# Kernel tuning notes

Hardware: AMD Instinct MI355X
Metric: run time of the kernel (lower is better)

Reference implementation:

```python
import jax, jax.numpy as jnp
import numpy as np

# ---- fixed wavelet filters (Selesnick FSfarras first-stage + Kingsbury Q-shift) ----
_F1 = np.array([
    [0.0, 0.0],
    [-0.08838834764832, -0.01122679215254],
    [0.08838834764832, 0.01122679215254],
    [0.69587998903400, 0.08838834764832],
    [0.69587998903400, 0.08838834764832],
    [0.08838834764832, -0.69587998903400],
    [-0.08838834764832, 0.69587998903400],
    [0.01122679215254, -0.08838834764832],
    [0.01122679215254, -0.08838834764832],
    [0.0, 0.0]], np.float32)
_F2 = np.array([
    [0.01122679215254, 0.0],
    [0.01122679215254, 0.0],
    [-0.08838834764832, -0.08838834764832],
    [0.08838834764832, -0.08838834764832],
    [0.69587998903400, 0.69587998903400],
    [0.69587998903400, -0.69587998903400],
    [0.08838834764832, 0.08838834764832],
    [-0.08838834764832, 0.08838834764832],
    [0.0, 0.01122679215254],
    [0.0, -0.01122679215254]], np.float32)
_Q1 = np.array([
    [0.03516384, 0.0],
    [0.0, 0.0],
    [-0.08832942, -0.11430184],
    [0.23389032, 0.0],
    [0.76027237, 0.58751830],
    [0.58751830, -0.76027237],
    [0.0, 0.23389032],
    [-0.11430184, 0.08832942],
    [0.0, 0.0],
    [0.0, -0.03516384]], np.float32)
_Q2 = np.array([
    [0.0, -0.03516384],
    [0.0, 0.0],
    [-0.11430184, 0.08832942],
    [0.0, 0.23389032],
    [0.58751830, -0.76027237],
    [0.76027237, 0.58751830],
    [0.23389032, 0.0],
    [-0.08832942, -0.11430184],
    [0.0, 0.0],
    [0.03516384, 0.0]], np.float32)
# synthesis filters are the time-reversed analysis filters
FSF = jnp.asarray(np.stack([_F1[::-1].copy(), _F2[::-1].copy()]))  # [2, 10, 2] first stage
SF = jnp.asarray(np.stack([_Q1[::-1].copy(), _Q2[::-1].copy()]))   # [2, 10, 2] Q-shift


def _upconv(x, f, axis):
    """Upsample-by-2 + full convolution with 1D filter f along `axis` (upfirdn(x,f,2,1))."""
    L = f.shape[0]
    xm = jnp.moveaxis(x, axis, -1)
    shp = xm.shape
    xr = xm.reshape(-1, 1, shp[-1])  # [M, 1, n] NCW
    k = f[::-1].astype(x.dtype).reshape(1, 1, L)  # flip -> true convolution
    y = jax.lax.conv_general_dilated(
        xr, k, window_strides=(1,), padding=[(L - 1, L - 1)],
        lhs_dilation=(2,), dimension_numbers=('NCW', 'OIW', 'NCW'))  # [M,1,2n+L-2]
    y = y.reshape(shp[:-1] + (y.shape[-1],))
    return jnp.moveaxis(y, -1, axis)


def sfb1d(lo, hi, sf, axis):
    """1D synthesis filter bank with periodic wrap + circular shift (Selesnick sfb1D)."""
    L = sf.shape[0]
    N = 2 * lo.shape[axis]
    y = _upconv(lo, sf[:, 0], axis) + _upconv(hi, sf[:, 1], axis)  # length N+L-2
    yN = jax.lax.slice_in_dim(y, 0, N, axis=axis)
    tail = jax.lax.slice_in_dim(y, N, N + L - 2, axis=axis)
    head = jax.lax.slice_in_dim(yN, 0, L - 2, axis=axis) + tail
    rest = jax.lax.slice_in_dim(yN, L - 2, N, axis=axis)
    return jnp.roll(jnp.concatenate([head, rest], axis=axis), 1 - L // 2, axis=axis)


def sfb2d(lo, hi3, sf_row, sf_col):
    """2D separable synthesis: hi3 = (LH, HL, HH); x is [B, H, W, C]."""
    lo = sfb1d(lo, hi3[0], sf_col, axis=2)
    h = sfb1d(hi3[1], hi3[2], sf_col, axis=2)
    return sfb1d(lo, h, sf_row, axis=1)


def _idtcwt(highs0, highs1, lows):
    inv_sqrt2 = jnp.asarray(1.0 / np.sqrt(2.0), highs0.dtype)

    def pm(a, b):
        return (a + b) * inv_sqrt2, (a - b) * inv_sqrt2

    # orientation butterflies per level (add_sub)
    wi = [[[[None] * 3 for _ in range(2)] for _ in range(2)] for _ in range(2)]
    for j, hj in enumerate((highs0, highs1)):
        for b in range(3):
            u, v = pm(hj[0, 0, b], hj[1, 1, b])
            wi[j][0][0][b], wi[j][1][1][b] = u, v
            u, v = pm(hj[0, 1, b], hj[1, 0, b])
            wi[j][0][1][b], wi[j][1][0][b] = u, v

    y = jnp.zeros_like(lows[0, 0], shape=(lows.shape[2], lows.shape[3] * 4,
                                          lows.shape[4] * 4, lows.shape[5]))
    for m in range(2):
        for n in range(2):
            lo = lows[m, n]
            lo = sfb2d(lo, wi[1][m][n], SF[m], SF[n])      # level 2 (Q-shift)
            lo = sfb2d(lo, wi[0][m][n], FSF[m], FSF[n])    # level 1 (first stage)
            y = y + lo
    return y / 2


def setup_inputs() -> dict:
    key = jax.random.key(0)
    k0, k1, k2 = jax.random.split(key, 3)
    B, C = 16, 3
    highs0 = jax.random.normal(k0, (2, 2, 3, B, 256, 256, C), dtype=jnp.float32)
    highs1 = jax.random.normal(k1, (2, 2, 3, B, 128, 128, C), dtype=jnp.float32)
    lows = jax.random.normal(k2, (2, 2, B, 128, 128, C), dtype=jnp.float32)
    return {"highs0": highs0, "highs1": highs1, "lows": lows}


def reference(highs0, highs1, lows):
    return _idtcwt(highs0, highs1, lows)
```

## Files before the change

kernel.cpp:

```cpp
#include <hip/hip_runtime.h>

#define INV_SQRT2 0.70710678118654752440f
#define KH 0.35355339059327376220f

constexpr float c_first[2][10][2] = {
  { { 0.00000000000000f,  0.00000000000000f},
    {-0.08838834764832f, -0.01122679215254f},
    { 0.08838834764832f,  0.01122679215254f},
    { 0.69587998903400f,  0.08838834764832f},
    { 0.69587998903400f,  0.08838834764832f},
    { 0.08838834764832f, -0.69587998903400f},
    {-0.08838834764832f,  0.69587998903400f},
    { 0.01122679215254f, -0.08838834764832f},
    { 0.01122679215254f, -0.08838834764832f},
    { 0.00000000000000f,  0.00000000000000f} },
  { { 0.01122679215254f,  0.00000000000000f},
    { 0.01122679215254f,  0.00000000000000f},
    {-0.08838834764832f, -0.08838834764832f},
    { 0.08838834764832f, -0.08838834764832f},
    { 0.69587998903400f,  0.69587998903400f},
    { 0.69587998903400f, -0.69587998903400f},
    { 0.08838834764832f,  0.08838834764832f},
    {-0.08838834764832f,  0.08838834764832f},
    { 0.00000000000000f,  0.01122679215254f},
    { 0.00000000000000f, -0.01122679215254f} }
};

__constant__ float c_qshift[2][10][2] = {
  { { 0.03516384f,  0.00000000f},
    { 0.00000000f,  0.00000000f},
    {-0.08832942f, -0.11430184f},
    { 0.23389032f,  0.00000000f},
    { 0.76027237f,  0.58751830f},
    { 0.58751830f, -0.76027237f},
    { 0.00000000f,  0.23389032f},
    {-0.11430184f,  0.08832942f},
    { 0.00000000f,  0.00000000f},
    { 0.00000000f, -0.03516384f} },
  { { 0.00000000f, -0.03516384f},
    { 0.00000000f,  0.00000000f},
    {-0.11430184f,  0.08832942f},
    { 0.00000000f,  0.23389032f},
    { 0.58751830f, -0.76027237f},
    { 0.76027237f,  0.58751830f},
    { 0.23389032f,  0.00000000f},
    {-0.08832942f, -0.11430184f},
    { 0.00000000f,  0.00000000f},
    { 0.03516384f,  0.00000000f} }
};

__global__ __launch_bounds__(128) void idtcwt_stage1(
    const float* __restrict__ lows, const float* __restrict__ highs1,
    float* __restrict__ lo2)
{
  constexpr int HIN = 128, WIN = 128, C = 3, B = 16;
  constexpr int ROWF  = WIN * C;
  constexpr int ROWO  = 2 * WIN * C;
  constexpr int PLANE = HIN * WIN * C;
  constexpr int SEG   = 16;

  const int jj = blockIdx.x * 128 + threadIdx.x;
  const int c  = jj % 3;
  const int t  = jj / 3;
  const int z  = blockIdx.z;
  const int combo = z >> 4;
  const int b     = z & 15;
  const int m = combo >> 1, n = combo & 1;

  const float* lo = lows + (combo * B + b) * PLANE;
  const int pa = (m == n) ? 0 : 1;
  const int pb = (m == n) ? 3 : 2;
  const float sgn = (m == 0) ? 1.0f : -1.0f;
  const int bandStride = B * PLANE;
  const float* hA = highs1 + (pa * 3 * B + b) * PLANE;
  const float* hB = highs1 + (pb * 3 * B + b) * PLANE;

  int wc3[5];
#pragma unroll
  for (int p = 0; p < 5; ++p) {
    int w = t + 2 - p;
    if (w >= WIN) w -= WIN;
    if (w < 0)  w += WIN;
    wc3[p] = w * C + c;
  }

  float lae[5], lao[5], hae[5], hao[5];
#pragma unroll
  for (int k = 0; k < 5; ++k) { lae[k]=0.f; lao[k]=0.f; hae[k]=0.f; hao[k]=0.f; }

  const int s0 = blockIdx.y * SEG;
  float* outp = lo2 + (combo * B + b) * (4 * PLANE);

#pragma unroll 1
  for (int ui = 0; ui < SEG + 4; ++ui) {
    const int u  = (s0 - 2 + ui) & (HIN - 1);
#pragma unroll
    for (int k = 0; k < 4; ++k) { lae[k]=lae[k+1]; lao[k]=lao[k+1]; hae[k]=hae[k+1]; hao[k]=hao[k+1]; }
    const int rb = u * ROWF;

    float rl[5], rA[3][5], rB[3][5];
#pragma unroll
    for (int p = 0; p < 5; ++p) {
      const int idx = rb + wc3[p];
      rl[p]    = lo[idx];
      rA[0][p] = hA[idx];
      rB[0][p] = hB[idx];
      rA[1][p] = hA[idx +   bandStride];
      rB[1][p] = hB[idx +   bandStride];
      rA[2][p] = hA[idx + 2*bandStride];
      rB[2][p] = hB[idx + 2*bandStride];
    }

    float aLe=0.f, aLo=0.f, aHe=0.f, aHo=0.f;
#pragma unroll
    for (int p = 0; p < 5; ++p) {
      const float lv  = rl[p];
      const float lhv = (rA[0][p] + sgn * rB[0][p]) * INV_SQRT2;
      const float hlv = (rA[1][p] + sgn * rB[1][p]) * INV_SQRT2;
      const float hhv = (rA[2][p] + sgn * rB[2][p]) * INV_SQRT2;
      const float ce0 = c_qshift[n][9 - 2*p][0], ce1 = c_qshift[n][9 - 2*p][1];
      const float co0 = c_qshift[n][8 - 2*p][0], co1 = c_qshift[n][8 - 2*p][1];
      aLe += ce0 * lv  + ce1 * lhv;
      aLo += co0 * lv  + co1 * lhv;
      aHe += ce0 * hlv + ce1 * hhv;
      aHo += co0 * hlv + co1 * hhv;
    }
    lae[4]=aLe; lao[4]=aLo; hae[4]=aHe; hao[4]=aHo;

    if (ui >= 4) {
      const int s = s0 + ui - 4;
      float o00=0.f, o01=0.f, o10=0.f, o11=0.f;
#pragma unroll
      for (int p = 0; p < 5; ++p) {
        const float f0l = c_qshift[m][9 - 2*p][0], f0h = c_qshift[m][9 - 2*p][1];
        const float f1l = c_qshift[m][8 - 2*p][0], f1h = c_qshift[m][8 - 2*p][1];
        o00 += f0l*lae[4-p] + f0h*hae[4-p];
        o01 += f0l*lao[4-p] + f0h*hao[4-p];
        o10 += f1l*lae[4-p] + f1h*hae[4-p];
        o11 += f1l*lao[4-p] + f1h*hao[4-p];
      }
      float* q = outp + (2*s) * ROWO + (2*t) * C + c;
      q[0]        = o00;
      q[C]        = o01;
      q[ROWO]     = o10;
      q[ROWO + C] = o11;
    }
  }
}

__global__ __launch_bounds__(256, 3) void idtcwt_stage2(
    const float* __restrict__ lo2, const float* __restrict__ highs0,
    float* __restrict__ out)
{
  constexpr int HIN = 256, WIN = 256, C = 3, B = 16;
  constexpr int ROWF  = WIN * C;
  constexpr int ROWO  = 2 * WIN * C;
  constexpr int PLANE = HIN * WIN * C;
  constexpr int OPLANE = 512 * 512 * C;
  constexpr int SEG   = 16;
  constexpr int NI    = SEG + 4;
  constexpr int PITCH = 5;
  constexpr int BUFV4 = 272 * PITCH;

  __shared__ float4 lds4[2 * BUFV4];

  const int tid = threadIdx.x;
  const int jj  = blockIdx.x * 256 + tid;
  const int c   = jj % 3;
  const int t   = jj / 3;
  const int b   = blockIdx.z;

  const int bandStride = B * PLANE;
  const float* a0  = lo2 + (0 * B + b) * PLANE;
  const float* a1  = lo2 + (1 * B + b) * PLANE;
  const float* a2  = lo2 + (2 * B + b) * PLANE;
  const float* a3  = lo2 + (3 * B + b) * PLANE;
  const float* h00b0 = highs0 + (0 * 3 * B + b) * PLANE;
  const float* h01b0 = highs0 + (1 * 3 * B + b) * PLANE;
  const float* h10b0 = highs0 + (2 * 3 * B + b) * PLANE;
  const float* h11b0 = highs0 + (3 * 3 * B + b) * PLANE;
  const float* h00b1 = h00b0 + bandStride;
  const float* h01b1 = h01b0 + bandStride;
  const float* h10b1 = h10b0 + bandStride;
  const float* h11b1 = h11b0 + bandStride;
  const float* h00b2 = h00b0 + 2*bandStride;
  const float* h01b2 = h01b0 + 2*bandStride;
  const float* h10b2 = h10b0 + 2*bandStride;
  const float* h11b2 = h11b0 + 2*bandStride;

  int j1 = jj - 6;   if (j1 < 0)     j1 += ROWF;
  int j2 = jj + 250; if (j2 >= ROWF) j2 -= ROWF;
  const bool halo = (tid < 12);

  float wla0e[5], wla0o[5], wla1e[5], wla1o[5];
  float wha0e[5], wha0o[5], wha1e[5], wha1o[5];

  const int s0 = blockIdx.y * SEG;
  float* outb = out + b * OPLANE;

  float4 G0, G1, G2, G3, Hh0, Hh1, Hh2, Hh3;

#define S2_LOAD(I)                                                           \
  {                                                                          \
    const int rb_ = ((s0 - 2 + (I)) & (HIN - 1)) * ROWF;                     \
    const int o1_ = rb_ + j1;                                                \
    G0 = make_float4(a0[o1_], a1[o1_], a2[o1_], a3[o1_]);                    \
    G1 = make_float4(h00b0[o1_], h11b0[o1_], h01b0[o1_], h10b0[o1_]);        \
    G2 = make_float4(h00b1[o1_], h11b1[o1_], h01b1[o1_], h10b1[o1_]);        \
    G3 = make_float4(h00b2[o1_], h11b2[o1_], h01b2[o1_], h10b2[o1_]);        \
    if (halo) {                                                              \
      const int o2_ = rb_ + j2;                                              \
      Hh0 = make_float4(a0[o2_], a1[o2_], a2[o2_], a3[o2_]);                 \
      Hh1 = make_float4(h00b0[o2_], h11b0[o2_], h01b0[o2_], h10b0[o2_]);     \
      Hh2 = make_float4(h00b1[o2_], h11b1[o2_], h01b1[o2_], h10b1[o2_]);     \
      Hh3 = make_float4(h00b2[o2_], h11b2[o2_], h01b2[o2_], h10b2[o2_]);     \
    }                                                                        \
  }

#define S2_WRITE(DST)                                                        \
  {                                                                          \
    float4* w_ = (DST) + tid * PITCH;                                        \
    w_[0] = make_float4(G0.x*0.5f, G0.y*0.5f, G0.z*0.5f, G0.w*0.5f);         \
    w_[1] = make_float4((G1.x+G1.y)*KH, (G1.x-G1.y)*KH,                      \
                        (G1.z+G1.w)*KH, (G1.z-G1.w)*KH);                     \
    w_[2] = make_float4((G2.x+G2.y)*KH, (G2.x-G2.y)*KH,                      \
                        (G2.z+G2.w)*KH, (G2.z-G2.w)*KH);                     \
    w_[3] = make_float4((G3.x+G3.y)*KH, (G3.x-G3.y)*KH,                      \
                        (G3.z+G3.w)*KH, (G3.z-G3.w)*KH);                     \
    if (halo) {                                                              \
      float4* w2_ = (DST) + (256 + tid) * PITCH;                             \
      w2_[0] = make_float4(Hh0.x*0.5f, Hh0.y*0.5f, Hh0.z*0.5f, Hh0.w*0.5f);  \
      w2_[1] = make_float4((Hh1.x+Hh1.y)*KH, (Hh1.x-Hh1.y)*KH,               \
                           (Hh1.z+Hh1.w)*KH, (Hh1.z-Hh1.w)*KH);              \
      w2_[2] = make_float4((Hh2.x+Hh2.y)*KH, (Hh2.x-Hh2.y)*KH,               \
                           (Hh2.z+Hh2.w)*KH, (Hh2.z-Hh2.w)*KH);              \
      w2_[3] = make_float4((Hh3.x+Hh3.y)*KH, (Hh3.x-Hh3.y)*KH,               \
                           (Hh3.z+Hh3.w)*KH, (Hh3.z-Hh3.w)*KH);              \
    }                                                                        \
  }

  float4* cur = lds4;
  float4* nxt = lds4 + BUFV4;

  S2_LOAD(0);
  S2_WRITE(cur);
  __syncthreads();

#pragma unroll 1
  for (int uo = 0; uo < 4; ++uo) {
#pragma unroll
    for (int k = 0; k < 5; ++k) {
      const int i = uo * 5 + k;

      if (i < NI - 1) {
        S2_LOAD(i + 1);
        __builtin_amdgcn_sched_barrier(0);
      }

      float A0e=0.f,A0o=0.f,A1e=0.f,A1o=0.f, H0e=0.f,H0o=0.f,H1e=0.f,H1o=0.f;
#pragma unroll
      for (int p = 0; p < 5; ++p) {
        const float4* qp = cur + (tid + (12 - 3*p)) * PITCH;
        const float4 q0 = qp[0], q1 = qp[1], q2 = qp[2], q3 = qp[3];
        const float a0e = c_first[0][9-2*p][0], a0o = c_first[0][8-2*p][0];
        const float b0e = c_first[0][9-2*p][1], b0o = c_first[0][8-2*p][1];
        const float a1e = c_first[1][9-2*p][0], a1o = c_first[1][8-2*p][0];
        const float b1e = c_first[1][9-2*p][1], b1o = c_first[1][8-2*p][1];
        A0e += a0e*q0.x + a1e*q0.y;   A0o += a0o*q0.x + a1o*q0.y;
        A1e += a0e*q0.z + a1e*q0.w;   A1o += a0o*q0.z + a1o*q0.w;
        A0e += b0e*q1.x + b1e*q1.z;   A0o += b0o*q1.x + b1o*q1.z;
        A1e += b0e*q1.w + b1e*q1.y;   A1o += b0o*q1.w + b1o*q1.y;
        H0e += a0e*q2.x + a1e*q2.z;   H0o += a0o*q2.x + a1o*q2.z;
        H1e += a0e*q2.w + a1e*q2.y;   H1o += a0o*q2.w + a1o*q2.y;
        H0e += b0e*q3.x + b1e*q3.z;   H0o += b0o*q3.x + b1o*q3.z;
        H1e += b0e*q3.w + b1e*q3.y;   H1o += b0o*q3.w + b1o*q3.y;
      }
      wla0e[k]=A0e; wla0o[k]=A0o; wla1e[k]=A1e; wla1o[k]=A1o;
      wha0e[k]=H0e; wha0o[k]=H0o; wha1e[k]=H1e; wha1o[k]=H1o;

      if (i >= 4) {
        const int s = s0 + i - 4;
        float o00=0.f, o01=0.f, o10=0.f, o11=0.f;
#pragma unroll
        for (int p = 0; p < 5; ++p) {
          const int kk = (k - p + 5) % 5;
          const float f00 = c_first[0][9-2*p][0], g00 = c_first[0][9-2*p][1];
          const float f01 = c_first[0][8-2*p][0], g01 = c_first[0][8-2*p][1];
          const float f10 = c_first[1][9-2*p][0], g10 = c_first[1][9-2*p][1];
          const float f11 = c_first[1][8-2*p][0], g11 = c_first[1][8-2*p][1];
          o00 += f00*wla0e[kk] + g00*wha0e[kk] + f10*wla1e[kk] + g10*wha1e[kk];
          o01 += f00*wla0o[kk] + g00*wha0o[kk] + f10*wla1o[kk] + g10*wha1o[kk];
          o10 += f01*wla0e[kk] + g01*wha0e[kk] + f11*wla1e[kk] + g11*wha1e[kk];
          o11 += f01*wla0o[kk] + g01*wha0o[kk] + f11*wla1o[kk] + g11*wha1o[kk];
        }
        float* q = outb + (2*s) * ROWO + (2*t) * C + c;
        q[0]        = o00;
        q[C]        = o01;
        q[ROWO]     = o10;
        q[ROWO + C] = o11;
      }

      if (i < NI - 1) {
        S2_WRITE(nxt);
      }
      __syncthreads();
      { float4* tmp = cur; cur = nxt; nxt = tmp; }
    }
  }
#undef S2_LOAD
#undef S2_WRITE
}

extern "C" void kernel_launch(void* const* d_in, const int* in_sizes, int n_in,
                              void* d_out, int out_size, void* d_ws, size_t ws_size,
                              hipStream_t stream) {
  const float* highs0 = (const float*)d_in[0];
  const float* highs1 = (const float*)d_in[1];
  const float* lows   = (const float*)d_in[2];
  float* out = (float*)d_out;
  float* lo2 = (float*)d_ws;

  dim3 b1(128), g1(3, 8, 64);
  hipLaunchKernelGGL(idtcwt_stage1, g1, b1, 0, stream, lows, highs1, lo2);

  dim3 b2(256), g2(3, 16, 16);
  hipLaunchKernelGGL(idtcwt_stage2, g2, b2, 0, stream, lo2, highs0, out);
}
```

Measured before the change: 109.0 us.

## Halve row segments, single-buffer LDS, and raise occupancy in both stages

Both kernels now process 8-row segments instead of 16, doubling the grid, and stage 2 drops its LDS double buffer for a single buffer with an extra barrier per row. The sliding window in stage 2 grows to 6 entries so it matches the 12-iteration loop. Launch bounds ask for more waves per SIMD, and empty asm statements in stage 1 force all global loads to issue before any math. The goal is more parallelism and occupancy to hide memory latency. The cost is more halo rows reloaded per segment and extra synchronisation.

After: 380.3 us. 249% more time.

```diff
diff --git a/kernel.cpp b/kernel.cpp
--- a/kernel.cpp
+++ b/kernel.cpp
@@ -49,7 +49,7 @@
     { 0.03516384f,  0.00000000f} }
 };
 
-__global__ __launch_bounds__(128) void idtcwt_stage1(
+__global__ __launch_bounds__(128, 4) void idtcwt_stage1(
     const float* __restrict__ lows, const float* __restrict__ highs1,
     float* __restrict__ lo2)
 {
@@ -57,7 +57,7 @@
   constexpr int ROWF  = WIN * C;
   constexpr int ROWO  = 2 * WIN * C;
   constexpr int PLANE = HIN * WIN * C;
-  constexpr int SEG   = 16;
+  constexpr int SEG   = 8;
 
   const int jj = blockIdx.x * 128 + threadIdx.x;
   const int c  = jj % 3;
@@ -110,6 +110,13 @@
       rA[2][p] = hA[idx + 2*bandStride];
       rB[2][p] = hB[idx + 2*bandStride];
     }
+    asm volatile("" :: "v"(rl[0]),"v"(rl[1]),"v"(rl[2]),"v"(rl[3]),"v"(rl[4]),
+                       "v"(rA[0][0]),"v"(rA[0][1]),"v"(rA[0][2]),"v"(rA[0][3]),"v"(rA[0][4]),
+                       "v"(rA[1][0]),"v"(rA[1][1]),"v"(rA[1][2]),"v"(rA[1][3]),"v"(rA[1][4]));
+    asm volatile("" :: "v"(rA[2][0]),"v"(rA[2][1]),"v"(rA[2][2]),"v"(rA[2][3]),"v"(rA[2][4]),
+                       "v"(rB[0][0]),"v"(rB[0][1]),"v"(rB[0][2]),"v"(rB[0][3]),"v"(rB[0][4]),
+                       "v"(rB[1][0]),"v"(rB[1][1]),"v"(rB[1][2]),"v"(rB[1][3]),"v"(rB[1][4]));
+    asm volatile("" :: "v"(rB[2][0]),"v"(rB[2][1]),"v"(rB[2][2]),"v"(rB[2][3]),"v"(rB[2][4]));
 
     float aLe=0.f, aLo=0.f, aHe=0.f, aHo=0.f;
 #pragma unroll
@@ -148,7 +155,7 @@
   }
 }
 
-__global__ __launch_bounds__(256, 3) void idtcwt_stage2(
+__global__ __launch_bounds__(256, 6) void idtcwt_stage2(
     const float* __restrict__ lo2, const float* __restrict__ highs0,
     float* __restrict__ out)
 {
@@ -157,12 +164,12 @@
   constexpr int ROWO  = 2 * WIN * C;
   constexpr int PLANE = HIN * WIN * C;
   constexpr int OPLANE = 512 * 512 * C;
-  constexpr int SEG   = 16;
+  constexpr int SEG   = 8;
   constexpr int NI    = SEG + 4;
   constexpr int PITCH = 5;
   constexpr int BUFV4 = 272 * PITCH;
 
-  __shared__ float4 lds4[2 * BUFV4];
+  __shared__ float4 lds4[BUFV4];
 
   const int tid = threadIdx.x;
   const int jj  = blockIdx.x * 256 + tid;
@@ -192,13 +199,19 @@
   int j2 = jj + 250; if (j2 >= ROWF) j2 -= ROWF;
   const bool halo = (tid < 12);
 
-  float wla0e[5], wla0o[5], wla1e[5], wla1o[5];
-  float wha0e[5], wha0o[5], wha1e[5], wha1o[5];
+  float wla0e[6], wla0o[6], wla1e[6], wla1o[6];
+  float wha0e[6], wha0o[6], wha1e[6], wha1o[6];
+#pragma unroll
+  for (int k = 0; k < 6; ++k) {
+    wla0e[k]=0.f; wla0o[k]=0.f; wla1e[k]=0.f; wla1o[k]=0.f;
+    wha0e[k]=0.f; wha0o[k]=0.f; wha1e[k]=0.f; wha1o[k]=0.f;
+  }
 
   const int s0 = blockIdx.y * SEG;
   float* outb = out + b * OPLANE;
 
-  float4 G0, G1, G2, G3, Hh0, Hh1, Hh2, Hh3;
+  float4 G0, G1, G2, G3;
+  float4 Hh0 = make_float4(0.f,0.f,0.f,0.f), Hh1 = Hh0, Hh2 = Hh0, Hh3 = Hh0;
 
 #define S2_LOAD(I)                                                           \
   {                                                                          \
@@ -217,9 +230,9 @@
     }                                                                        \
   }
 
-#define S2_WRITE(DST)                                                        \
+#define S2_WRITE()                                                           \
   {                                                                          \
-    float4* w_ = (DST) + tid * PITCH;                                        \
+    float4* w_ = lds4 + tid * PITCH;                                         \
     w_[0] = make_float4(G0.x*0.5f, G0.y*0.5f, G0.z*0.5f, G0.w*0.5f);         \
     w_[1] = make_float4((G1.x+G1.y)*KH, (G1.x-G1.y)*KH,                      \
                         (G1.z+G1.w)*KH, (G1.z-G1.w)*KH);                     \
@@ -228,7 +241,7 @@
     w_[3] = make_float4((G3.x+G3.y)*KH, (G3.x-G3.y)*KH,                      \
                         (G3.z+G3.w)*KH, (G3.z-G3.w)*KH);                     \
     if (halo) {                                                              \
-      float4* w2_ = (DST) + (256 + tid) * PITCH;                             \
+      float4* w2_ = lds4 + (256 + tid) * PITCH;                              \
       w2_[0] = make_float4(Hh0.x*0.5f, Hh0.y*0.5f, Hh0.z*0.5f, Hh0.w*0.5f);  \
       w2_[1] = make_float4((Hh1.x+Hh1.y)*KH, (Hh1.x-Hh1.y)*KH,               \
                            (Hh1.z+Hh1.w)*KH, (Hh1.z-Hh1.w)*KH);              \
@@ -239,18 +252,15 @@
     }                                                                        \
   }
 
-  float4* cur = lds4;
-  float4* nxt = lds4 + BUFV4;
-
   S2_LOAD(0);
-  S2_WRITE(cur);
+  S2_WRITE();
   __syncthreads();
 
 #pragma unroll 1
-  for (int uo = 0; uo < 4; ++uo) {
-#pragma unroll
-    for (int k = 0; k < 5; ++k) {
-      const int i = uo * 5 + k;
+  for (int uo = 0; uo < 2; ++uo) {
+#pragma unroll
+    for (int k = 0; k < 6; ++k) {
+      const int i = uo * 6 + k;
 
       if (i < NI - 1) {
         S2_LOAD(i + 1);
@@ -260,7 +270,7 @@
       float A0e=0.f,A0o=0.f,A1e=0.f,A1o=0.f, H0e=0.f,H0o=0.f,H1e=0.f,H1o=0.f;
 #pragma unroll
       for (int p = 0; p < 5; ++p) {
-        const float4* qp = cur + (tid + (12 - 3*p)) * PITCH;
+        const float4* qp = lds4 + (tid + (12 - 3*p)) * PITCH;
         const float4 q0 = qp[0], q1 = qp[1], q2 = qp[2], q3 = qp[3];
         const float a0e = c_first[0][9-2*p][0], a0o = c_first[0][8-2*p][0];
         const float b0e = c_first[0][9-2*p][1], b0o = c_first[0][8-2*p][1];
@@ -283,7 +293,7 @@
         float o00=0.f, o01=0.f, o10=0.f, o11=0.f;
 #pragma unroll
         for (int p = 0; p < 5; ++p) {
-          const int kk = (k - p + 5) % 5;
+          const int kk = (k - p + 6) % 6;
           const float f00 = c_first[0][9-2*p][0], g00 = c_first[0][9-2*p][1];
           const float f01 = c_first[0][8-2*p][0], g01 = c_first[0][8-2*p][1];
           const float f10 = c_first[1][9-2*p][0], g10 = c_first[1][9-2*p][1];
@@ -300,11 +310,11 @@
         q[ROWO + C] = o11;
       }
 
+      __syncthreads();
       if (i < NI - 1) {
-        S2_WRITE(nxt);
+        S2_WRITE();
       }
       __syncthreads();
-      { float4* tmp = cur; cur = nxt; nxt = tmp; }
     }
   }
 #undef S2_LOAD
@@ -320,9 +330,9 @@
   float* out = (float*)d_out;
   float* lo2 = (float*)d_ws;
 
-  dim3 b1(128), g1(3, 8, 64);
+  dim3 b1(128), g1(3, 16, 64);
   hipLaunchKernelGGL(idtcwt_stage1, g1, b1, 0, stream, lows, highs1, lo2);
 
-  dim3 b2(256), g2(3, 16, 16);
+  dim3 b2(256), g2(3, 32, 16);
   hipLaunchKernelGGL(idtcwt_stage2, g2, b2, 0, stream, lo2, highs0, out);
 }
```
